# Optimization experiments

Measured on AMD Instinct MI355X. Metric: run time of the kernel, lower is better.

The kernel has to match this reference:

```python
import jax, jax.numpy as jnp
import numpy as np

D_MODEL = 1024
N_HEADS = 16
D_K = D_MODEL // N_HEADS
THETA = 10000.0
MAX_SEQ_LEN = 2048


def _rope_tables(seq_len):
    pos = jnp.arange(seq_len, dtype=jnp.float32)
    inv_freq = 1.0 / (THETA ** (jnp.arange(0, D_K, 2, dtype=jnp.float32) / D_K))
    ang = pos[:, None] * inv_freq[None, :]  # [T, D_K/2]
    return jnp.cos(ang), jnp.sin(ang)


def _apply_rope(x, cos, sin):
    # x: [..., T, D_K]; cos/sin: [T, D_K/2]
    x_even = x[..., ::2]
    x_odd = x[..., 1::2]
    r_even = x_even * cos - x_odd * sin
    r_odd = x_even * sin + x_odd * cos
    out = jnp.stack([r_even, r_odd], axis=-1)  # [..., T, D_K/2, 2]
    return out.reshape(x.shape)


def setup_inputs() -> dict:
    key = jax.random.key(0)
    ks = jax.random.split(key, 5)
    std = np.sqrt(2.0 / (D_MODEL + D_MODEL))
    x = jax.random.normal(ks[0], (2, 2048, D_MODEL), dtype=jnp.float32)
    w_q = jax.random.normal(ks[1], (D_MODEL, D_MODEL), dtype=jnp.float32) * std
    w_k = jax.random.normal(ks[2], (D_MODEL, D_MODEL), dtype=jnp.float32) * std
    w_v = jax.random.normal(ks[3], (D_MODEL, D_MODEL), dtype=jnp.float32) * std
    w_o = jax.random.normal(ks[4], (D_MODEL, D_MODEL), dtype=jnp.float32) * std
    return {"x": x, "w_q": w_q, "w_k": w_k, "w_v": w_v, "w_o": w_o}


def reference(x, w_q, w_k, w_v, w_o):
    B, T, _ = x.shape
    # projections: weight stored as [d_out, d_in], y = x @ W^T
    q = jnp.einsum('btd,od->bto', x, w_q)
    k = jnp.einsum('btd,od->bto', x, w_k)
    v = jnp.einsum('btd,od->bto', x, w_v)
    # split heads: [B, T, H*Dk] -> [B, H, T, Dk]
    q = q.reshape(B, T, N_HEADS, D_K).transpose(0, 2, 1, 3)
    k = k.reshape(B, T, N_HEADS, D_K).transpose(0, 2, 1, 3)
    v = v.reshape(B, T, N_HEADS, D_K).transpose(0, 2, 1, 3)
    cos, sin = _rope_tables(T)
    q = _apply_rope(q, cos, sin)
    k = _apply_rope(k, cos, sin)
    scores = jnp.einsum('bhqd,bhkd->bhqk', q, k) / np.sqrt(D_K).astype(np.float32)
    causal = jnp.tril(jnp.ones((T, T), dtype=bool))
    scores = jnp.where(causal, scores, -jnp.inf)
    attn = jax.nn.softmax(scores, axis=-1)
    out = jnp.einsum('bhqk,bhkd->bhqd', attn, v)
    out = out.transpose(0, 2, 1, 3).reshape(B, T, D_MODEL)
    return jnp.einsum('btd,od->bto', out, w_o)
```

## Files before the change

kernel.cpp:

```cpp
#include <hip/hip_runtime.h>
#include <hip/hip_bf16.h>

typedef __bf16 bf16_t;
typedef __bf16 bf16x8 __attribute__((ext_vector_type(8)));
typedef float f32x4 __attribute__((ext_vector_type(4)));
typedef short short4v __attribute__((ext_vector_type(4)));

#define D_MODEL 1024
#define T_SEQ 2048
#define NH 16
#define DKD 64
#define X_ELEMS (4194304u)
#define W_ELEMS (1048576u)
#define Q_SCALE 0.18033688011112042f

__device__ __forceinline__ void async16(const bf16_t* g, bf16_t* l) {
    __builtin_amdgcn_global_load_lds((const __attribute__((address_space(1))) void*)g,
                                     (__attribute__((address_space(3))) void*)l, 16, 0, 0);
}

__global__ __launch_bounds__(256) void convert_kernel(
    const float* __restrict__ x, const float* __restrict__ wq,
    const float* __restrict__ wk, const float* __restrict__ wv,
    const float* __restrict__ wo,
    bf16_t* __restrict__ xb, bf16_t* __restrict__ wqb, bf16_t* __restrict__ wkb,
    bf16_t* __restrict__ wvb, bf16_t* __restrict__ wob)
{
    size_t idx = ((size_t)blockIdx.x * 256 + threadIdx.x) * 4;
    const float* src; bf16_t* dst; size_t off;
    if (idx < X_ELEMS) { src = x; dst = xb; off = idx; }
    else {
        size_t r = idx - X_ELEMS;
        unsigned w = (unsigned)(r >> 20);
        off = r & (W_ELEMS - 1);
        src = (w == 0) ? wq : (w == 1) ? wk : (w == 2) ? wv : wo;
        dst = (w == 0) ? wqb : (w == 1) ? wkb : (w == 2) ? wvb : wob;
    }
    float4 v = *(const float4*)(src + off);
    union { bf16_t b[4]; short4v s; } u;
    u.b[0] = (bf16_t)v.x; u.b[1] = (bf16_t)v.y;
    u.b[2] = (bf16_t)v.z; u.b[3] = (bf16_t)v.w;
    *(short4v*)(dst + off) = u.s;
}

__global__ __launch_bounds__(256) void rope_kernel(float* __restrict__ cost, float* __restrict__ sint)
{
    int idx = blockIdx.x * 256 + threadIdx.x;
    int t = idx >> 5, i = idx & 31;
    float inv = expf(-0.28782313662425572f * (float)i);
    float ang = (float)t * inv;
    float s, c;
    sincosf(ang, &s, &c);
    cost[idx] = c; sint[idx] = s;
}

__global__ __launch_bounds__(256) void gemm_fused(
    const bf16_t* __restrict__ A,
    const bf16_t* __restrict__ W0, const bf16_t* __restrict__ W1, const bf16_t* __restrict__ W2,
    bf16_t* __restrict__ qout, bf16_t* __restrict__ kout, bf16_t* __restrict__ vout,
    const float* __restrict__ cost, const float* __restrict__ sint,
    float* __restrict__ fout, float* __restrict__ fpart, int modeBase)
{
    __shared__ bf16_t As[128 * 32];
    __shared__ bf16_t Bs[128 * 32];
    const int tid = threadIdx.x;
    const int wave = tid >> 6, lane = tid & 63;
    const int quad = lane >> 4, l16 = lane & 15;
    const int m0 = blockIdx.x * 128;
    const int n0 = blockIdx.y * 128;
    const int wm = (wave >> 1) * 64, wn = (wave & 1) * 64;
    const int mode = (modeBase == 3) ? 3 : (modeBase + blockIdx.z);
    const int kz = (modeBase == 3) ? blockIdx.z : 0;
    const int kBeg = kz * 512;
    const int kEnd = (modeBase == 3) ? (kBeg + 512) : 1024;
    const bf16_t* W = (mode == 1) ? W1 : (mode == 2) ? W2 : W0;

    const bf16_t* Afrag = (mode == 2) ? Bs : As;
    const bf16_t* Bfrag = (mode == 2) ? As : Bs;
    const int aoff = (mode == 2) ? wn : wm;
    const int boff = (mode == 2) ? wm : wn;

    const f32x4 fzero = {0.f, 0.f, 0.f, 0.f};
    f32x4 acc[4][4];
    #pragma unroll
    for (int i = 0; i < 4; ++i)
        #pragma unroll
        for (int j = 0; j < 4; ++j) acc[i][j] = fzero;

    for (int k0 = kBeg; k0 < kEnd; k0 += 32) {
        __syncthreads();
        #pragma unroll
        for (int c = 0; c < 2; ++c) {
            int G = c * 256 + tid;
            int row = G >> 2, go = G & 3;
            async16(A + (size_t)(m0 + row) * 1024 + (k0 + go * 8), As + (size_t)(c * 256 + wave * 64) * 8);
            async16(W + (size_t)(n0 + row) * 1024 + (k0 + go * 8), Bs + (size_t)(c * 256 + wave * 64) * 8);
        }
        __syncthreads();
        bf16x8 af[4], bfv[4];
        #pragma unroll
        for (int mi = 0; mi < 4; ++mi)
            af[mi] = *(const bf16x8*)(Afrag + (aoff + mi * 16 + l16) * 32 + quad * 8);
        #pragma unroll
        for (int ni = 0; ni < 4; ++ni)
            bfv[ni] = *(const bf16x8*)(Bfrag + (boff + ni * 16 + l16) * 32 + quad * 8);
        #pragma unroll
        for (int mi = 0; mi < 4; ++mi)
            #pragma unroll
            for (int ni = 0; ni < 4; ++ni)
                acc[mi][ni] = __builtin_amdgcn_mfma_f32_16x16x32_bf16(af[mi], bfv[ni], acc[mi][ni], 0, 0, 0);
    }

    #pragma unroll
    for (int mi = 0; mi < 4; ++mi) {
        #pragma unroll
        for (int ni = 0; ni < 4; ++ni) {
            #pragma unroll
            for (int reg = 0; reg < 4; ++reg) {
                float v = acc[mi][ni][reg];
                if (mode == 2) {
                    int f   = n0 + wn + mi * 16 + quad * 4 + reg;
                    int tok = m0 + wm + ni * 16 + l16;
                    int t = tok & (T_SEQ - 1), b = tok >> 11;
                    int h = f >> 6, dk = f & 63;
                    vout[(((size_t)b * NH + h) * DKD + dk) * T_SEQ + t] = (bf16_t)v;
                } else {
                    int row = m0 + wm + mi * 16 + quad * 4 + reg;
                    int col = n0 + wn + ni * 16 + l16;
                    if (mode == 3) {
                        float* fo = kz ? fpart : fout;
                        fo[(size_t)row * D_MODEL + col] = v;
                    } else {
                        int t = row & (T_SEQ - 1), b = row >> 11;
                        int h = col >> 6, dk = col & 63;
                        float vp = __shfl_xor(v, 1);
                        int fi = dk >> 1;
                        float c = cost[t * 32 + fi], s = sint[t * 32 + fi];
                        float r = (dk & 1) ? (vp * s + v * c) : (v * c - vp * s);
                        if (mode == 0) r *= Q_SCALE;
                        bf16_t* dst = (mode == 0) ? qout : kout;
                        dst[(((size_t)b * NH + h) * T_SEQ + t) * DKD + dk] = (bf16_t)r;
                    }
                }
            }
        }
    }
}

__global__ __launch_bounds__(256) void add_kernel(float* __restrict__ out, const float* __restrict__ part)
{
    size_t i = ((size_t)blockIdx.x * 256 + threadIdx.x) * 4;
    float4 o = *(const float4*)(out + i);
    float4 p = *(const float4*)(part + i);
    o.x += p.x; o.y += p.y; o.z += p.z; o.w += p.w;
    *(float4*)(out + i) = o;
}

__global__ __launch_bounds__(256, 2) void attn_kernel(
    const bf16_t* __restrict__ Q, const bf16_t* __restrict__ Kb,
    const bf16_t* __restrict__ Vt, bf16_t* __restrict__ O)
{
    __shared__ float Ocomb[3][2][4][4][16][4];
    __shared__ float Lcomb[3][2][64];
    __shared__ bf16_t Pw[4][16 * 72];
    const int tid = threadIdx.x;
    const int wave = tid >> 6, lane = tid & 63;
    const int quad = lane >> 4, l16 = lane & 15;
    const int bh = blockIdx.x;
    const int qb = 63 - (int)blockIdx.y;
    const int qw = qb * 32;

    const bf16_t* kbase = Kb + (size_t)bh * T_SEQ * DKD;
    const bf16_t* vbase = Vt + (size_t)bh * DKD * T_SEQ;

    bf16x8 qf[2][2];
    #pragma unroll
    for (int j = 0; j < 2; ++j) {
        const bf16_t* qp = Q + ((size_t)bh * T_SEQ + qw + j * 16 + l16) * DKD;
        qf[j][0] = *(const bf16x8*)(qp + quad * 8);
        qf[j][1] = *(const bf16x8*)(qp + 32 + quad * 8);
    }
    const f32x4 fzero = {0.f, 0.f, 0.f, 0.f};
    f32x4 oacc[2][4];
    #pragma unroll
    for (int j = 0; j < 2; ++j)
        #pragma unroll
        for (int i = 0; i < 4; ++i) oacc[j][i] = fzero;
    float lsum[2] = {0.f, 0.f};

    const int nkt = (qw + 95) >> 6;

    bf16x8 kcur[4][2], knxt[4][2], vcur[4][2];
    #pragma unroll
    for (int fi = 0; fi < 4; ++fi) {
        const bf16_t* kr = kbase + (size_t)(wave * 64 + fi * 16 + l16) * DKD + quad * 8;
        kcur[fi][0] = *(const bf16x8*)(kr);
        kcur[fi][1] = *(const bf16x8*)(kr + 32);
    }

    for (int kt = wave; kt < nkt; kt += 4) {
        const int k0 = kt * 64;
        #pragma unroll
        for (int di = 0; di < 4; ++di) {
            const bf16_t* vr = vbase + (size_t)(di * 16 + l16) * T_SEQ + k0 + quad * 8;
            vcur[di][0] = *(const bf16x8*)(vr);
            vcur[di][1] = *(const bf16x8*)(vr + 32);
        }
        if (kt + 4 < nkt) {
            #pragma unroll
            for (int fi = 0; fi < 4; ++fi) {
                const bf16_t* kr = kbase + (size_t)((kt + 4) * 64 + fi * 16 + l16) * DKD + quad * 8;
                knxt[fi][0] = *(const bf16x8*)(kr);
                knxt[fi][1] = *(const bf16x8*)(kr + 32);
            }
        }

        #pragma unroll
        for (int j = 0; j < 2; ++j) {
            if (k0 > qw + j * 16 + 15) continue;
            const int qcol = qw + j * 16 + l16;
            f32x4 s[4];
            #pragma unroll
            for (int fi = 0; fi < 4; ++fi) {
                f32x4 z = fzero;
                z = __builtin_amdgcn_mfma_f32_16x16x32_bf16(kcur[fi][0], qf[j][0], z, 0, 0, 0);
                z = __builtin_amdgcn_mfma_f32_16x16x32_bf16(kcur[fi][1], qf[j][1], z, 0, 0, 0);
                s[fi] = z;
            }
            if (k0 + 63 > qw + j * 16) {
                #pragma unroll
                for (int fi = 0; fi < 4; ++fi)
                    #pragma unroll
                    for (int reg = 0; reg < 4; ++reg) {
                        int key = k0 + fi * 16 + quad * 4 + reg;
                        s[fi][reg] = (key > qcol) ? -__builtin_inff() : s[fi][reg];
                    }
            }
            float sm = 0.f;
            #pragma unroll
            for (int fi = 0; fi < 4; ++fi)
                #pragma unroll
                for (int reg = 0; reg < 4; ++reg) {
                    float p = __builtin_amdgcn_exp2f(s[fi][reg]);
                    s[fi][reg] = p;
                    sm += p;
                }
            lsum[j] += sm;

            bf16_t* pw = &Pw[wave][0];
            #pragma unroll
            for (int fi = 0; fi < 4; ++fi) {
                union { bf16_t h[4]; unsigned long long u64; } pk;
                pk.h[0] = (bf16_t)s[fi][0]; pk.h[1] = (bf16_t)s[fi][1];
                pk.h[2] = (bf16_t)s[fi][2]; pk.h[3] = (bf16_t)s[fi][3];
                *(unsigned long long*)(pw + l16 * 72 + fi * 16 + quad * 4) = pk.u64;
            }
            bf16x8 pf[2];
            pf[0] = *(const bf16x8*)(pw + l16 * 72 + quad * 8);
            pf[1] = *(const bf16x8*)(pw + l16 * 72 + 32 + quad * 8);

            #pragma unroll
            for (int di = 0; di < 4; ++di) {
                oacc[j][di] = __builtin_amdgcn_mfma_f32_16x16x32_bf16(vcur[di][0], pf[0], oacc[j][di], 0, 0, 0);
                oacc[j][di] = __builtin_amdgcn_mfma_f32_16x16x32_bf16(vcur[di][1], pf[1], oacc[j][di], 0, 0, 0);
            }
        }

        if (kt + 4 < nkt) {
            #pragma unroll
            for (int fi = 0; fi < 4; ++fi) {
                kcur[fi][0] = knxt[fi][0];
                kcur[fi][1] = knxt[fi][1];
            }
        }
    }

    if (wave > 0) {
        #pragma unroll
        for (int j = 0; j < 2; ++j) {
            #pragma unroll
            for (int di = 0; di < 4; ++di)
                *(f32x4*)&Ocomb[wave - 1][j][di][quad][l16][0] = oacc[j][di];
            Lcomb[wave - 1][j][lane] = lsum[j];
        }
    }
    __syncthreads();
    if (wave != 0) return;

    #pragma unroll
    for (int j = 0; j < 2; ++j) {
        #pragma unroll
        for (int w = 0; w < 3; ++w) {
            #pragma unroll
            for (int di = 0; di < 4; ++di) {
                f32x4 p = *(const f32x4*)&Ocomb[w][j][di][quad][l16][0];
                #pragma unroll
                for (int reg = 0; reg < 4; ++reg) oacc[j][di][reg] += p[reg];
            }
            lsum[j] += Lcomb[w][j][lane];
        }
    }

    const int b = bh >> 4, h = bh & 15;
    #pragma unroll
    for (int j = 0; j < 2; ++j) {
        float l = lsum[j];
        l += __shfl_xor(l, 16);
        l += __shfl_xor(l, 32);
        float rl = 1.0f / l;
        int q = qw + j * 16 + l16;
        #pragma unroll
        for (int di = 0; di < 4; ++di) {
            union { bf16_t hh[4]; unsigned long long u64; } ok;
            #pragma unroll
            for (int reg = 0; reg < 4; ++reg) ok.hh[reg] = (bf16_t)(oacc[j][di][reg] * rl);
            int d = di * 16 + quad * 4;
            *(unsigned long long*)(O + ((size_t)b * T_SEQ + q) * D_MODEL + h * DKD + d) = ok.u64;
        }
    }
}

extern "C" void kernel_launch(void* const* d_in, const int* in_sizes, int n_in,
                              void* d_out, int out_size, void* d_ws, size_t ws_size,
                              hipStream_t stream)
{
    const float* x  = (const float*)d_in[0];
    const float* wq = (const float*)d_in[1];
    const float* wk = (const float*)d_in[2];
    const float* wv = (const float*)d_in[3];
    const float* wo = (const float*)d_in[4];
    float* out = (float*)d_out;

    char* ws = (char*)d_ws;
    size_t off = 0;
    auto alloc = [&](size_t bytes) -> void* {
        void* p = ws + off; off += (bytes + 255) & ~(size_t)255; return p;
    };
    bf16_t* xb   = (bf16_t*)alloc((size_t)X_ELEMS * 2);
    bf16_t* wqb  = (bf16_t*)alloc((size_t)W_ELEMS * 2);
    bf16_t* wkb  = (bf16_t*)alloc((size_t)W_ELEMS * 2);
    bf16_t* wvb  = (bf16_t*)alloc((size_t)W_ELEMS * 2);
    bf16_t* wob  = (bf16_t*)alloc((size_t)W_ELEMS * 2);
    bf16_t* qb   = (bf16_t*)alloc((size_t)X_ELEMS * 2);
    bf16_t* kb   = (bf16_t*)alloc((size_t)X_ELEMS * 2);
    bf16_t* vtb  = (bf16_t*)alloc((size_t)X_ELEMS * 2);
    bf16_t* ob   = (bf16_t*)alloc((size_t)X_ELEMS * 2);
    float*  cost = (float*)alloc((size_t)T_SEQ * 32 * 4);
    float*  sint = (float*)alloc((size_t)T_SEQ * 32 * 4);
    float*  fpart = (float*)qb;

    convert_kernel<<<8192, 256, 0, stream>>>(x, wq, wk, wv, wo, xb, wqb, wkb, wvb, wob);
    rope_kernel<<<256, 256, 0, stream>>>(cost, sint);
    gemm_fused<<<dim3(32, 8, 3), 256, 0, stream>>>(xb, wqb, wkb, wvb, qb, kb, vtb, cost, sint,
                                                   nullptr, nullptr, 0);
    attn_kernel<<<dim3(32, 64), 256, 0, stream>>>(qb, kb, vtb, ob);
    gemm_fused<<<dim3(32, 8, 2), 256, 0, stream>>>(ob, wob, nullptr, nullptr, nullptr, nullptr, nullptr,
                                                   cost, sint, out, fpart, 3);
    add_kernel<<<4096, 256, 0, stream>>>(out, fpart);
}
```

Measured before the change: 227.7 us.

## Use BK=64 swizzled LDS tiles and drop split-K in output GEMM

The GEMM K-tile grows from 32 to 64, halving the number of barrier pairs per K loop. An XOR swizzle on the 16-byte chunk index is added to the LDS layout so the wider rows avoid bank conflicts on fragment reads. The output projection no longer splits K in two, which removes the partial-sum buffer and the separate add kernel, but it also halves that GEMM's grid to 256 blocks. A per-mode device function with two specialized kernels replaces the runtime mode dispatch. LDS per block doubles, which may reduce occupancy.

New measurement: 226.6 us. Within noise of the previous version (-0.5%).

```diff
diff --git a/kernel.cpp b/kernel.cpp
--- a/kernel.cpp
+++ b/kernel.cpp
@@ -54,26 +54,21 @@
     cost[idx] = c; sint[idx] = s;
 }
 
-__global__ __launch_bounds__(256) void gemm_fused(
-    const bf16_t* __restrict__ A,
-    const bf16_t* __restrict__ W0, const bf16_t* __restrict__ W1, const bf16_t* __restrict__ W2,
+__device__ __forceinline__ void gemm_body(
+    int mode,
+    const bf16_t* __restrict__ A, const bf16_t* __restrict__ W,
     bf16_t* __restrict__ qout, bf16_t* __restrict__ kout, bf16_t* __restrict__ vout,
     const float* __restrict__ cost, const float* __restrict__ sint,
-    float* __restrict__ fout, float* __restrict__ fpart, int modeBase)
-{
-    __shared__ bf16_t As[128 * 32];
-    __shared__ bf16_t Bs[128 * 32];
+    float* __restrict__ fout)
+{
+    __shared__ bf16_t As[128 * 64];
+    __shared__ bf16_t Bs[128 * 64];
     const int tid = threadIdx.x;
     const int wave = tid >> 6, lane = tid & 63;
     const int quad = lane >> 4, l16 = lane & 15;
     const int m0 = blockIdx.x * 128;
     const int n0 = blockIdx.y * 128;
     const int wm = (wave >> 1) * 64, wn = (wave & 1) * 64;
-    const int mode = (modeBase == 3) ? 3 : (modeBase + blockIdx.z);
-    const int kz = (modeBase == 3) ? blockIdx.z : 0;
-    const int kBeg = kz * 512;
-    const int kEnd = (modeBase == 3) ? (kBeg + 512) : 1024;
-    const bf16_t* W = (mode == 1) ? W1 : (mode == 2) ? W2 : W0;
 
     const bf16_t* Afrag = (mode == 2) ? Bs : As;
     const bf16_t* Bfrag = (mode == 2) ? As : Bs;
@@ -87,28 +82,36 @@
         #pragma unroll
         for (int j = 0; j < 4; ++j) acc[i][j] = fzero;
 
-    for (int k0 = kBeg; k0 < kEnd; k0 += 32) {
+    for (int k0 = 0; k0 < 1024; k0 += 64) {
         __syncthreads();
         #pragma unroll
-        for (int c = 0; c < 2; ++c) {
+        for (int c = 0; c < 4; ++c) {
             int G = c * 256 + tid;
-            int row = G >> 2, go = G & 3;
+            int row = G >> 3, p = G & 7;
+            int go = p ^ (row & 7);
             async16(A + (size_t)(m0 + row) * 1024 + (k0 + go * 8), As + (size_t)(c * 256 + wave * 64) * 8);
             async16(W + (size_t)(n0 + row) * 1024 + (k0 + go * 8), Bs + (size_t)(c * 256 + wave * 64) * 8);
         }
         __syncthreads();
-        bf16x8 af[4], bfv[4];
-        #pragma unroll
-        for (int mi = 0; mi < 4; ++mi)
-            af[mi] = *(const bf16x8*)(Afrag + (aoff + mi * 16 + l16) * 32 + quad * 8);
-        #pragma unroll
-        for (int ni = 0; ni < 4; ++ni)
-            bfv[ni] = *(const bf16x8*)(Bfrag + (boff + ni * 16 + l16) * 32 + quad * 8);
-        #pragma unroll
-        for (int mi = 0; mi < 4; ++mi)
-            #pragma unroll
-            for (int ni = 0; ni < 4; ++ni)
-                acc[mi][ni] = __builtin_amdgcn_mfma_f32_16x16x32_bf16(af[mi], bfv[ni], acc[mi][ni], 0, 0, 0);
+        #pragma unroll
+        for (int ks = 0; ks < 2; ++ks) {
+            bf16x8 af[4], bfv[4];
+            #pragma unroll
+            for (int mi = 0; mi < 4; ++mi) {
+                int r = aoff + mi * 16 + l16;
+                af[mi] = *(const bf16x8*)(Afrag + r * 64 + (((ks * 4 + quad) ^ (r & 7)) * 8));
+            }
+            #pragma unroll
+            for (int ni = 0; ni < 4; ++ni) {
+                int r = boff + ni * 16 + l16;
+                bfv[ni] = *(const bf16x8*)(Bfrag + r * 64 + (((ks * 4 + quad) ^ (r & 7)) * 8));
+            }
+            #pragma unroll
+            for (int mi = 0; mi < 4; ++mi)
+                #pragma unroll
+                for (int ni = 0; ni < 4; ++ni)
+                    acc[mi][ni] = __builtin_amdgcn_mfma_f32_16x16x32_bf16(af[mi], bfv[ni], acc[mi][ni], 0, 0, 0);
+        }
     }
 
     #pragma unroll
@@ -128,8 +131,7 @@
                     int row = m0 + wm + mi * 16 + quad * 4 + reg;
                     int col = n0 + wn + ni * 16 + l16;
                     if (mode == 3) {
-                        float* fo = kz ? fpart : fout;
-                        fo[(size_t)row * D_MODEL + col] = v;
+                        fout[(size_t)row * D_MODEL + col] = v;
                     } else {
                         int t = row & (T_SEQ - 1), b = row >> 11;
                         int h = col >> 6, dk = col & 63;
@@ -147,13 +149,22 @@
     }
 }
 
-__global__ __launch_bounds__(256) void add_kernel(float* __restrict__ out, const float* __restrict__ part)
-{
-    size_t i = ((size_t)blockIdx.x * 256 + threadIdx.x) * 4;
-    float4 o = *(const float4*)(out + i);
-    float4 p = *(const float4*)(part + i);
-    o.x += p.x; o.y += p.y; o.z += p.z; o.w += p.w;
-    *(float4*)(out + i) = o;
+__global__ __launch_bounds__(256) void gemm_qkv(
+    const bf16_t* __restrict__ A,
+    const bf16_t* __restrict__ W0, const bf16_t* __restrict__ W1, const bf16_t* __restrict__ W2,
+    bf16_t* __restrict__ qout, bf16_t* __restrict__ kout, bf16_t* __restrict__ vout,
+    const float* __restrict__ cost, const float* __restrict__ sint)
+{
+    const int mode = blockIdx.z;
+    const bf16_t* W = (mode == 1) ? W1 : (mode == 2) ? W2 : W0;
+    gemm_body(mode, A, W, qout, kout, vout, cost, sint, nullptr);
+}
+
+__global__ __launch_bounds__(256) void gemm_out(
+    const bf16_t* __restrict__ A, const bf16_t* __restrict__ W,
+    float* __restrict__ fout)
+{
+    gemm_body(3, A, W, nullptr, nullptr, nullptr, nullptr, nullptr, fout);
 }
 
 __global__ __launch_bounds__(256, 2) void attn_kernel(
@@ -347,14 +358,10 @@
     bf16_t* ob   = (bf16_t*)alloc((size_t)X_ELEMS * 2);
     float*  cost = (float*)alloc((size_t)T_SEQ * 32 * 4);
     float*  sint = (float*)alloc((size_t)T_SEQ * 32 * 4);
-    float*  fpart = (float*)qb;
 
     convert_kernel<<<8192, 256, 0, stream>>>(x, wq, wk, wv, wo, xb, wqb, wkb, wvb, wob);
     rope_kernel<<<256, 256, 0, stream>>>(cost, sint);
-    gemm_fused<<<dim3(32, 8, 3), 256, 0, stream>>>(xb, wqb, wkb, wvb, qb, kb, vtb, cost, sint,
-                                                   nullptr, nullptr, 0);
+    gemm_qkv<<<dim3(32, 8, 3), 256, 0, stream>>>(xb, wqb, wkb, wvb, qb, kb, vtb, cost, sint);
     attn_kernel<<<dim3(32, 64), 256, 0, stream>>>(qb, kb, vtb, ob);
-    gemm_fused<<<dim3(32, 8, 2), 256, 0, stream>>>(ob, wob, nullptr, nullptr, nullptr, nullptr, nullptr,
-                                                   cost, sint, out, fpart, 3);
-    add_kernel<<<4096, 256, 0, stream>>>(out, fpart);
-}
+    gemm_out<<<dim3(32, 8, 1), 256, 0, stream>>>(ob, wob, out);
+}
```
